# Optimization experiments

Hardware: AMD Instinct MI355X
Metric: run time of the kernel (lower is better)

## Reference

```python
import jax, jax.numpy as jnp
import numpy as np

D_MODEL = 1024
N_HEADS = 16
HEAD_DIM = D_MODEL // N_HEADS


def setup_inputs() -> dict:
    key = jax.random.key(0)
    k1, k2, k3, k4, k5 = jax.random.split(key, 5)
    s = 1.0 / np.sqrt(D_MODEL)
    return {
        "x": jax.random.normal(k1, (2, 2048, D_MODEL), dtype=jnp.float32),
        "w_qkv": jax.random.normal(k2, (D_MODEL, 3 * D_MODEL), dtype=jnp.float32) * s,
        "b_qkv": jax.random.normal(k3, (3 * D_MODEL,), dtype=jnp.float32) * 0.02,
        "w_proj": jax.random.normal(k4, (D_MODEL, D_MODEL), dtype=jnp.float32) * s,
        "b_proj": jax.random.normal(k5, (D_MODEL,), dtype=jnp.float32) * 0.02,
    }


def reference(x, w_qkv, b_qkv, w_proj, b_proj):
    B, S, D = x.shape
    H, Hd = N_HEADS, HEAD_DIM
    qkv = x @ w_qkv + b_qkv                       # [B,S,3D]
    q, k, v = jnp.split(qkv, 3, axis=-1)
    # split heads -> [B,H,S,Hd]
    q = q.reshape(B, S, H, Hd).transpose(0, 2, 1, 3)
    k = k.reshape(B, S, H, Hd).transpose(0, 2, 1, 3)
    v = v.reshape(B, S, H, Hd).transpose(0, 2, 1, 3)
    scale = 1.0 / jnp.sqrt(jnp.asarray(Hd, dtype=x.dtype))
    scores = jnp.einsum("bhqd,bhkd->bhqk", q, k) * scale  # [B,H,S,S]
    causal = jnp.tril(jnp.ones((S, S), dtype=bool))
    scores = jnp.where(causal, scores, jnp.asarray(-jnp.inf, dtype=scores.dtype))
    attn = jax.nn.softmax(scores, axis=-1)
    out = jnp.einsum("bhqk,bhkd->bhqd", attn, v)  # [B,H,S,Hd]
    out = out.transpose(0, 2, 1, 3).reshape(B, S, D)
    return out @ w_proj + b_proj
```

## Files before the change

kernel.cpp:

```cpp
#include <hip/hip_runtime.h>


typedef float f32x4 __attribute__((ext_vector_type(4)));
typedef short bf16x8 __attribute__((ext_vector_type(8)));

#if __has_builtin(__builtin_amdgcn_exp2f)
#define EXP2(x) __builtin_amdgcn_exp2f(x)
#else
#define EXP2(x) exp2f(x)
#endif

__device__ __forceinline__ unsigned short f2bf(float f) {
  union { float f; unsigned u; } v; v.f = f;
  unsigned u = v.u + 0x7fffu + ((v.u >> 16) & 1u);
  return (unsigned short)(u >> 16);
}

__device__ __forceinline__ unsigned pack2bf(float f0, float f1) {
  union { float f; unsigned u; } a, b;
  a.f = f1; b.f = f0;
  return __builtin_amdgcn_perm(a.u + 0x8000u, b.u + 0x8000u, 0x07060302u);
}

__device__ __forceinline__ void async_load16(const void* g, void* lds) {
  __builtin_amdgcn_global_load_lds(
      (const __attribute__((address_space(1))) void*)g,
      (__attribute__((address_space(3))) void*)lds, 16, 0, 0);
}

__global__ void f32_to_bf16_kernel(const float* __restrict__ in,
                                   unsigned short* __restrict__ out, int n) {
  int i = (blockIdx.x * 256 + threadIdx.x) * 4;
  if (i < n) {
    float4 f = *(const float4*)(in + i);
    ushort4 o;
    o.x = f2bf(f.x); o.y = f2bf(f.y); o.z = f2bf(f.z); o.w = f2bf(f.w);
    *(ushort4*)(out + i) = o;
  }
}

__global__ void transpose_f32_bf16_kernel(const float* __restrict__ in,
                                          unsigned short* __restrict__ out,
                                          int K, int N) {
  __shared__ float tile[32][33];
  int n0 = blockIdx.x * 32, k0 = blockIdx.y * 32;
  int tx = threadIdx.x, ty = threadIdx.y;
#pragma unroll
  for (int i = ty; i < 32; i += 8)
    tile[i][tx] = in[(size_t)(k0 + i) * N + (n0 + tx)];
  __syncthreads();
#pragma unroll
  for (int i = ty; i < 32; i += 8)
    out[(size_t)(n0 + i) * K + (k0 + tx)] = f2bf(tile[tx][i]);
}

template <int MI, int NI>
__device__ __forceinline__ void gemm_mainloop(
    const unsigned short* __restrict__ A,
    const unsigned short* __restrict__ BT,
    int K, int mBlk, int nBlk,
    unsigned short* As, unsigned short* Bs,
    f32x4 (&acc)[MI][NI], int lane, int wave)
{
  const int l16 = lane & 15, quad = lane >> 4;
  const int mW = (wave >> 1) * MI * 16;
  const int nW = (wave & 1) * NI * 16;
  constexpr int AROWS = 2 * MI * 16;
  constexpr int BROWS = 2 * NI * 16;
  constexpr int AINST = AROWS / 64;
  constexpr int BINST = BROWS / 64;
  const int rl = lane >> 2;
  const int cl = (lane & 3) * 8;

  for (int k0 = 0; k0 < K; k0 += 32) {
    __syncthreads();
#pragma unroll
    for (int t = 0; t < AINST; ++t) {
      const int rbase = wave * (AROWS / 4) + t * 16;
      async_load16(A + (size_t)(mBlk + rbase + rl) * K + k0 + cl, &As[rbase * 32]);
    }
#pragma unroll
    for (int t = 0; t < BINST; ++t) {
      const int rbase = wave * (BROWS / 4) + t * 16;
      async_load16(BT + (size_t)(nBlk + rbase + rl) * K + k0 + cl, &Bs[rbase * 32]);
    }
    __syncthreads();

    bf16x8 af[MI], bf[NI];
#pragma unroll
    for (int i = 0; i < MI; ++i)
      af[i] = *(const bf16x8*)&As[(mW + i * 16 + l16) * 32 + quad * 8];
#pragma unroll
    for (int j = 0; j < NI; ++j)
      bf[j] = *(const bf16x8*)&Bs[(nW + j * 16 + l16) * 32 + quad * 8];
#pragma unroll
    for (int i = 0; i < MI; ++i)
#pragma unroll
      for (int j = 0; j < NI; ++j)
        acc[i][j] = __builtin_amdgcn_mfma_f32_16x16x32_bf16(af[i], bf[j], acc[i][j], 0, 0, 0);
  }
}

__global__ __launch_bounds__(256) void qkv_gemm_kernel(
    const unsigned short* __restrict__ A,
    const unsigned short* __restrict__ WT,
    const float* __restrict__ bias,
    unsigned short* __restrict__ QKV)
{
  __shared__ unsigned short As[128 * 32];
  __shared__ unsigned short Bs[128 * 32];
  const int lane = threadIdx.x & 63;
  const int wave = threadIdx.x >> 6;
  const int l16 = lane & 15, quad = lane >> 4;

  f32x4 acc[4][4];
  const f32x4 z4 = {0.f, 0.f, 0.f, 0.f};
#pragma unroll
  for (int i = 0; i < 4; ++i)
#pragma unroll
    for (int j = 0; j < 4; ++j) acc[i][j] = z4;

  gemm_mainloop<4, 4>(A, WT, 1024, blockIdx.x * 128, blockIdx.y * 128,
                      As, Bs, acc, lane, wave);

  const int m0 = blockIdx.x * 128 + (wave >> 1) * 64;
  const int n0 = blockIdx.y * 128 + (wave & 1) * 64;
  const int whichW = n0 >> 10;
  const int bb = m0 >> 11;
  const int sBase = (m0 & 2047);
  const size_t planeE = (size_t)2 * 16 * 2048 * 64;

  if (whichW == 2) {
    unsigned short* Vb = QKV + 2 * planeE;
#pragma unroll
    for (int j = 0; j < 4; ++j) {
      const int rem = (n0 & 1023) + j * 16 + l16;
      const int hh = rem >> 6, hd = rem & 63;
      const float bv = bias[n0 + j * 16 + l16];
      unsigned short* col = Vb + (((size_t)bb * 16 + hh) * 64 + hd) * 2048;
#pragma unroll
      for (int i = 0; i < 4; ++i) {
        unsigned short pk[4];
#pragma unroll
        for (int r = 0; r < 4; ++r) pk[r] = f2bf(acc[i][j][r] + bv);
        *(ushort4*)&col[sBase + i * 16 + quad * 4] = *(ushort4*)pk;
      }
    }
  } else {
    const float scale = (whichW == 0) ? 0.18033688011112042f : 1.0f;
#pragma unroll
    for (int j = 0; j < 4; ++j) {
      const int n = n0 + j * 16 + l16;
      const float bv = bias[n];
      const int rem = n & 1023;
      const int hh = rem >> 6, hd = rem & 63;
      unsigned short* pl = QKV + (size_t)whichW * planeE +
                           (((size_t)bb * 16 + hh) * 2048) * 64 + hd;
#pragma unroll
      for (int r = 0; r < 4; ++r) {
        const int s = sBase + (quad * 4 + r);
#pragma unroll
        for (int i = 0; i < 4; ++i)
          pl[(size_t)(s + i * 16) * 64] = f2bf((acc[i][j][r] + bv) * scale);
      }
    }
  }
}

__global__ __launch_bounds__(256) void attn_kernel(
    const unsigned short* __restrict__ QKV,
    unsigned short* __restrict__ AO)
{
  __shared__ __align__(16) unsigned short Ks[3 * 64 * 64];
  __shared__ __align__(16) unsigned short Vs[3 * 64 * 64];
  __shared__ unsigned short Plds[4 * 32 * 72];
  const int lane = threadIdx.x & 63;
  const int wave = threadIdx.x >> 6;
  const int l16 = lane & 15, quad = lane >> 4;
  const int h = blockIdx.y, b = blockIdx.z;
  const int qg = b ? blockIdx.x : (15 - blockIdx.x);
  const int qw = qg * 128 + wave * 32;

  const size_t planeE = (size_t)2 * 16 * 2048 * 64;
  const size_t bhS = ((size_t)b * 16 + h) * (size_t)(2048 * 64);
  const unsigned short* Q   = QKV + bhS;
  const unsigned short* Kg  = QKV + planeE + bhS;
  const unsigned short* VTg = QKV + 2 * planeE + bhS;

  unsigned short* Pw = Plds + wave * (32 * 72);
  const f32x4 z4 = {0.f, 0.f, 0.f, 0.f};

  bf16x8 qf_[2][2];
#pragma unroll
  for (int qf = 0; qf < 2; ++qf)
#pragma unroll
    for (int hf = 0; hf < 2; ++hf)
      qf_[qf][hf] = *(const bf16x8*)(Q + (size_t)(qw + qf * 16 + l16) * 64 + hf * 32 + quad * 8);

  f32x4 O[2][4];
#pragma unroll
  for (int qf = 0; qf < 2; ++qf)
#pragma unroll
    for (int f = 0; f < 4; ++f) O[qf][f] = z4;
  float lpa[2] = {0.f, 0.f}, lpb[2] = {0.f, 0.f};

  const int tbase = (wave & 1) * 4;
  const bool doV = wave >= 2;
  const int sw7 = l16 & 7;

  auto stage = [&](int tileIdx, int bufIdx) {
    const int kt = tileIdx * 64;
    unsigned short* Kb = Ks + bufIdx * 4096;
    unsigned short* Vb = Vs + bufIdx * 4096;
#pragma unroll
    for (int i = 0; i < 4; ++i) {
      const int t = tbase + i;
      const int s = t * 64 + lane;
      const int row = s >> 3;
      const int c = (s & 7) ^ (row & 7);
      if (doV)
        async_load16(VTg + (size_t)row * 2048 + kt + c * 8, Vb + t * 512);
      else
        async_load16(Kg + (size_t)(kt + row) * 64 + c * 8, Kb + t * 512);
    }
  };

  const int nt = qg * 2 + 2;
  stage(0, 0);
  stage(1, 1);
  for (int ti = 0; ti < nt; ++ti) {
    asm volatile("s_waitcnt vmcnt(4)\n\ts_barrier" ::: "memory");
    const int tn = (ti + 2 < nt) ? ti + 2 : nt - 1;
    stage(tn, (ti + 2) % 3);
    const int kt = ti * 64;
    const unsigned short* Kb = Ks + (ti % 3) * 4096;
    const unsigned short* Vb = Vs + (ti % 3) * 4096;

    if (kt <= qw + 31) {
      const bool dmask = (kt + 63 > qw);
      f32x4 sc[4][2];
#pragma unroll
      for (int kg = 0; kg < 4; ++kg) {
        const int row = kg * 16 + l16;
        bf16x8 ka0 = *(const bf16x8*)&Kb[(row * 8 + (quad ^ sw7)) * 8];
        bf16x8 ka1 = *(const bf16x8*)&Kb[(row * 8 + ((4 + quad) ^ sw7)) * 8];
#pragma unroll
        for (int qf = 0; qf < 2; ++qf) {
          f32x4 s0 = z4;
          s0 = __builtin_amdgcn_mfma_f32_16x16x32_bf16(ka0, qf_[qf][0], s0, 0, 0, 0);
          s0 = __builtin_amdgcn_mfma_f32_16x16x32_bf16(ka1, qf_[qf][1], s0, 0, 0, 0);
          sc[kg][qf] = s0;
        }
      }

#pragma unroll
      for (int kg = 0; kg < 4; ++kg)
#pragma unroll
        for (int qf = 0; qf < 2; ++qf) {
          float p[4];
#pragma unroll
          for (int r = 0; r < 4; ++r) {
            float v = sc[kg][qf][r];
            if (dmask) {
              const int key = kt + kg * 16 + quad * 4 + r;
              const int q = qw + qf * 16 + l16;
              if (key > q) v = -INFINITY;
            }
            p[r] = EXP2(v);
          }
          lpa[qf] += p[0] + p[1];
          lpb[qf] += p[2] + p[3];
          uint2 pk;
          pk.x = pack2bf(p[0], p[1]);
          pk.y = pack2bf(p[2], p[3]);
          *(uint2*)&Pw[(qf * 16 + l16) * 72 + kg * 16 + quad * 4] = pk;
        }
      asm volatile("s_waitcnt lgkmcnt(0)" ::: "memory");

#pragma unroll
      for (int ks = 0; ks < 2; ++ks) {
        bf16x8 pa[2];
#pragma unroll
        for (int qf = 0; qf < 2; ++qf)
          pa[qf] = *(const bf16x8*)&Pw[(qf * 16 + l16) * 72 + ks * 32 + quad * 8];
#pragma unroll
        for (int f = 0; f < 4; ++f) {
          const int row = f * 16 + l16;
          bf16x8 vb = *(const bf16x8*)&Vb[(row * 8 + ((ks * 4 + quad) ^ sw7)) * 8];
#pragma unroll
          for (int qf = 0; qf < 2; ++qf)
            O[qf][f] = __builtin_amdgcn_mfma_f32_16x16x32_bf16(pa[qf], vb, O[qf][f], 0, 0, 0);
        }
      }
    }
  }

  float lp[2] = {lpa[0] + lpb[0], lpa[1] + lpb[1]};
#pragma unroll
  for (int qf = 0; qf < 2; ++qf) {
    lp[qf] += __shfl_xor(lp[qf], 16, 64);
    lp[qf] += __shfl_xor(lp[qf], 32, 64);
  }

#pragma unroll
  for (int qf = 0; qf < 2; ++qf) {
    float inv[4];
#pragma unroll
    for (int r = 0; r < 4; ++r)
      inv[r] = 1.0f / __shfl(lp[qf], quad * 4 + r, 64);
    unsigned short* op = AO + ((size_t)b * 2048 + qw + qf * 16 + quad * 4) * 1024 + h * 64 + l16;
#pragma unroll
    for (int f = 0; f < 4; ++f)
#pragma unroll
      for (int r = 0; r < 4; ++r)
        op[(size_t)r * 1024 + f * 16] = f2bf(O[qf][f][r] * inv[r]);
  }
}

__global__ __launch_bounds__(256) void proj_gemm_kernel(
    const unsigned short* __restrict__ A,
    const unsigned short* __restrict__ WT,
    const float* __restrict__ bias,
    float* __restrict__ out)
{
  __shared__ unsigned short As[64 * 32];
  __shared__ unsigned short Bs[128 * 32];
  const int lane = threadIdx.x & 63;
  const int wave = threadIdx.x >> 6;
  const int l16 = lane & 15, quad = lane >> 4;

  f32x4 acc[2][4];
  const f32x4 z4 = {0.f, 0.f, 0.f, 0.f};
#pragma unroll
  for (int i = 0; i < 2; ++i)
#pragma unroll
    for (int j = 0; j < 4; ++j) acc[i][j] = z4;

  gemm_mainloop<2, 4>(A, WT, 1024, blockIdx.x * 64, blockIdx.y * 128,
                      As, Bs, acc, lane, wave);

  const int m0 = blockIdx.x * 64 + (wave >> 1) * 32;
  const int n0 = blockIdx.y * 128 + (wave & 1) * 64;
#pragma unroll
  for (int i = 0; i < 2; ++i) {
#pragma unroll
    for (int j = 0; j < 4; ++j) {
      const int n = n0 + j * 16 + l16;
      const float bv = bias[n];
#pragma unroll
      for (int r = 0; r < 4; ++r) {
        const int m = m0 + i * 16 + quad * 4 + r;
        out[(size_t)m * 1024 + n] = acc[i][j][r] + bv;
      }
    }
  }
}

extern "C" void kernel_launch(void* const* d_in, const int* in_sizes, int n_in,
                              void* d_out, int out_size, void* d_ws, size_t ws_size,
                              hipStream_t stream) {
  const float* x      = (const float*)d_in[0];
  const float* w_qkv  = (const float*)d_in[1];
  const float* b_qkv  = (const float*)d_in[2];
  const float* w_proj = (const float*)d_in[3];
  const float* b_proj = (const float*)d_in[4];
  float* out = (float*)d_out;

  unsigned short* Xb  = (unsigned short*)d_ws;
  unsigned short* WTq = Xb + (size_t)4096 * 1024;
  unsigned short* WTp = WTq + (size_t)3072 * 1024;
  unsigned short* QKV = WTp + (size_t)1024 * 1024;
  unsigned short* AO  = QKV + (size_t)3 * 4096 * 1024;

  f32_to_bf16_kernel<<<4096, 256, 0, stream>>>(x, Xb, 4096 * 1024);
  transpose_f32_bf16_kernel<<<dim3(96, 32), dim3(32, 8), 0, stream>>>(w_qkv, WTq, 1024, 3072);
  transpose_f32_bf16_kernel<<<dim3(32, 32), dim3(32, 8), 0, stream>>>(w_proj, WTp, 1024, 1024);
  qkv_gemm_kernel<<<dim3(32, 24), 256, 0, stream>>>(Xb, WTq, b_qkv, QKV);
  attn_kernel<<<dim3(16, 16, 2), 256, 0, stream>>>(QKV, AO);
  proj_gemm_kernel<<<dim3(64, 8), 256, 0, stream>>>(AO, WTp, b_proj, out);
}
```

Baseline: 204.0 us.

## Rewrite attention inner loop with 32x32 MFMA, register-resident P via permlane swap

The attention kernel now uses 32x32x16 bf16 MFMAs instead of 16x16x32 for both the QK^T scores and the PV accumulation. The probability tile is converted with v_cvt_pk_bf16_f32 and rearranged across lanes with v_permlane32_swap, so it no longer round-trips through an LDS scratch buffer. The softmax denominator is accumulated by an extra MFMA against a ones vector rather than scalar adds and shuffles, and s_setprio plus launch_bounds(256,2) are added. This removes LDS traffic and a wait per tile, at the cost of an extra MFMA per key chunk and higher register pressure from the 16-wide accumulators.

```diff
diff --git a/kernel.cpp b/kernel.cpp
--- a/kernel.cpp
+++ b/kernel.cpp
@@ -2,6 +2,7 @@
 
 
 typedef float f32x4 __attribute__((ext_vector_type(4)));
+typedef float f32x16 __attribute__((ext_vector_type(16)));
 typedef short bf16x8 __attribute__((ext_vector_type(8)));
 
 #if __has_builtin(__builtin_amdgcn_exp2f)
@@ -14,12 +15,6 @@
   union { float f; unsigned u; } v; v.f = f;
   unsigned u = v.u + 0x7fffu + ((v.u >> 16) & 1u);
   return (unsigned short)(u >> 16);
-}
-
-__device__ __forceinline__ unsigned pack2bf(float f0, float f1) {
-  union { float f; unsigned u; } a, b;
-  a.f = f1; b.f = f0;
-  return __builtin_amdgcn_perm(a.u + 0x8000u, b.u + 0x8000u, 0x07060302u);
 }
 
 __device__ __forceinline__ void async_load16(const void* g, void* lds) {
@@ -167,16 +162,16 @@
   }
 }
 
-__global__ __launch_bounds__(256) void attn_kernel(
+__global__ __launch_bounds__(256, 2) void attn_kernel(
     const unsigned short* __restrict__ QKV,
     unsigned short* __restrict__ AO)
 {
   __shared__ __align__(16) unsigned short Ks[3 * 64 * 64];
   __shared__ __align__(16) unsigned short Vs[3 * 64 * 64];
-  __shared__ unsigned short Plds[4 * 32 * 72];
   const int lane = threadIdx.x & 63;
   const int wave = threadIdx.x >> 6;
-  const int l16 = lane & 15, quad = lane >> 4;
+  const int l31 = lane & 31;
+  const int hi  = lane >> 5;
   const int h = blockIdx.y, b = blockIdx.z;
   const int qg = b ? blockIdx.x : (15 - blockIdx.x);
   const int qw = qg * 128 + wave * 32;
@@ -187,26 +182,21 @@
   const unsigned short* Kg  = QKV + planeE + bhS;
   const unsigned short* VTg = QKV + 2 * planeE + bhS;
 
-  unsigned short* Pw = Plds + wave * (32 * 72);
-  const f32x4 z4 = {0.f, 0.f, 0.f, 0.f};
-
-  bf16x8 qf_[2][2];
-#pragma unroll
-  for (int qf = 0; qf < 2; ++qf)
-#pragma unroll
-    for (int hf = 0; hf < 2; ++hf)
-      qf_[qf][hf] = *(const bf16x8*)(Q + (size_t)(qw + qf * 16 + l16) * 64 + hf * 32 + quad * 8);
-
-  f32x4 O[2][4];
-#pragma unroll
-  for (int qf = 0; qf < 2; ++qf)
-#pragma unroll
-    for (int f = 0; f < 4; ++f) O[qf][f] = z4;
-  float lpa[2] = {0.f, 0.f}, lpb[2] = {0.f, 0.f};
+  bf16x8 qf_[4];
+#pragma unroll
+  for (int t = 0; t < 4; ++t)
+    qf_[t] = *(const bf16x8*)(Q + (size_t)(qw + l31) * 64 + t * 16 + hi * 8);
+
+  bf16x8 onesf;
+#pragma unroll
+  for (int i = 0; i < 8; ++i) onesf[i] = (short)0x3F80;
+
+  f32x16 O[2], Osum;
+#pragma unroll
+  for (int r = 0; r < 16; ++r) { O[0][r] = 0.f; O[1][r] = 0.f; Osum[r] = 0.f; }
 
   const int tbase = (wave & 1) * 4;
   const bool doV = wave >= 2;
-  const int sw7 = l16 & 7;
 
   auto stage = [&](int tileIdx, int bufIdx) {
     const int kt = tileIdx * 64;
@@ -238,82 +228,72 @@
 
     if (kt <= qw + 31) {
       const bool dmask = (kt + 63 > qw);
-      f32x4 sc[4][2];
-#pragma unroll
-      for (int kg = 0; kg < 4; ++kg) {
-        const int row = kg * 16 + l16;
-        bf16x8 ka0 = *(const bf16x8*)&Kb[(row * 8 + (quad ^ sw7)) * 8];
-        bf16x8 ka1 = *(const bf16x8*)&Kb[(row * 8 + ((4 + quad) ^ sw7)) * 8];
-#pragma unroll
-        for (int qf = 0; qf < 2; ++qf) {
-          f32x4 s0 = z4;
-          s0 = __builtin_amdgcn_mfma_f32_16x16x32_bf16(ka0, qf_[qf][0], s0, 0, 0, 0);
-          s0 = __builtin_amdgcn_mfma_f32_16x16x32_bf16(ka1, qf_[qf][1], s0, 0, 0, 0);
-          sc[kg][qf] = s0;
+#pragma unroll
+      for (int kg = 0; kg < 2; ++kg) {
+        const int krow = kg * 32 + l31;
+        const int ks7 = krow & 7;
+        bf16x8 ka[4];
+#pragma unroll
+        for (int t = 0; t < 4; ++t)
+          ka[t] = *(const bf16x8*)&Kb[(krow * 8 + ((t * 2 + hi) ^ ks7)) * 8];
+
+        f32x16 sc;
+#pragma unroll
+        for (int r = 0; r < 16; ++r) sc[r] = 0.f;
+        __builtin_amdgcn_s_setprio(1);
+#pragma unroll
+        for (int t = 0; t < 4; ++t)
+          sc = __builtin_amdgcn_mfma_f32_32x32x16_bf16(ka[t], qf_[t], sc, 0, 0, 0);
+        __builtin_amdgcn_s_setprio(0);
+
+        float p[16];
+#pragma unroll
+        for (int r = 0; r < 16; ++r) {
+          float v = sc[r];
+          if (dmask) {
+            const int key = kt + kg * 32 + (r & 3) + 8 * (r >> 2) + 4 * hi;
+            if (key > qw + l31) v = -INFINITY;
+          }
+          p[r] = EXP2(v);
+        }
+        unsigned c8[8];
+#pragma unroll
+        for (int i = 0; i < 8; ++i)
+          asm("v_cvt_pk_bf16_f32 %0, %1, %2"
+              : "=v"(c8[i]) : "v"(p[2 * i]), "v"(p[2 * i + 1]));
+
+#pragma unroll
+        for (int half = 0; half < 2; ++half) {
+          unsigned a0 = c8[4 * half + 0], a1 = c8[4 * half + 1];
+          unsigned a2 = c8[4 * half + 2], a3 = c8[4 * half + 3];
+          asm("v_permlane32_swap_b32 %0, %1" : "+v"(a0), "+v"(a2));
+          asm("v_permlane32_swap_b32 %0, %1" : "+v"(a1), "+v"(a3));
+          union { unsigned u[4]; bf16x8 v; } pa;
+          pa.u[0] = a0; pa.u[1] = a1; pa.u[2] = a2; pa.u[3] = a3;
+          const int kc = kg * 2 + half;
+
+          __builtin_amdgcn_s_setprio(1);
+          Osum = __builtin_amdgcn_mfma_f32_32x32x16_bf16(pa.v, onesf, Osum, 0, 0, 0);
+#pragma unroll
+          for (int g = 0; g < 2; ++g) {
+            const int vrow = g * 32 + l31;
+            bf16x8 vb = *(const bf16x8*)&Vb[(vrow * 8 + ((kc * 2 + hi) ^ (vrow & 7))) * 8];
+            O[g] = __builtin_amdgcn_mfma_f32_32x32x16_bf16(pa.v, vb, O[g], 0, 0, 0);
+          }
+          __builtin_amdgcn_s_setprio(0);
         }
       }
-
-#pragma unroll
-      for (int kg = 0; kg < 4; ++kg)
-#pragma unroll
-        for (int qf = 0; qf < 2; ++qf) {
-          float p[4];
-#pragma unroll
-          for (int r = 0; r < 4; ++r) {
-            float v = sc[kg][qf][r];
-            if (dmask) {
-              const int key = kt + kg * 16 + quad * 4 + r;
-              const int q = qw + qf * 16 + l16;
-              if (key > q) v = -INFINITY;
-            }
-            p[r] = EXP2(v);
-          }
-          lpa[qf] += p[0] + p[1];
-          lpb[qf] += p[2] + p[3];
-          uint2 pk;
-          pk.x = pack2bf(p[0], p[1]);
-          pk.y = pack2bf(p[2], p[3]);
-          *(uint2*)&Pw[(qf * 16 + l16) * 72 + kg * 16 + quad * 4] = pk;
-        }
-      asm volatile("s_waitcnt lgkmcnt(0)" ::: "memory");
-
-#pragma unroll
-      for (int ks = 0; ks < 2; ++ks) {
-        bf16x8 pa[2];
-#pragma unroll
-        for (int qf = 0; qf < 2; ++qf)
-          pa[qf] = *(const bf16x8*)&Pw[(qf * 16 + l16) * 72 + ks * 32 + quad * 8];
-#pragma unroll
-        for (int f = 0; f < 4; ++f) {
-          const int row = f * 16 + l16;
-          bf16x8 vb = *(const bf16x8*)&Vb[(row * 8 + ((ks * 4 + quad) ^ sw7)) * 8];
-#pragma unroll
-          for (int qf = 0; qf < 2; ++qf)
-            O[qf][f] = __builtin_amdgcn_mfma_f32_16x16x32_bf16(pa[qf], vb, O[qf][f], 0, 0, 0);
-        }
-      }
-    }
-  }
-
-  float lp[2] = {lpa[0] + lpb[0], lpa[1] + lpb[1]};
-#pragma unroll
-  for (int qf = 0; qf < 2; ++qf) {
-    lp[qf] += __shfl_xor(lp[qf], 16, 64);
-    lp[qf] += __shfl_xor(lp[qf], 32, 64);
-  }
-
-#pragma unroll
-  for (int qf = 0; qf < 2; ++qf) {
-    float inv[4];
-#pragma unroll
-    for (int r = 0; r < 4; ++r)
-      inv[r] = 1.0f / __shfl(lp[qf], quad * 4 + r, 64);
-    unsigned short* op = AO + ((size_t)b * 2048 + qw + qf * 16 + quad * 4) * 1024 + h * 64 + l16;
-#pragma unroll
-    for (int f = 0; f < 4; ++f)
-#pragma unroll
-      for (int r = 0; r < 4; ++r)
-        op[(size_t)r * 1024 + f * 16] = f2bf(O[qf][f][r] * inv[r]);
+    }
+  }
+
+  unsigned short* base = AO + ((size_t)b * 2048 + qw) * 1024 + h * 64 + l31;
+#pragma unroll
+  for (int r = 0; r < 16; ++r) {
+    const float inv = 1.0f / Osum[r];
+    const int row = (r & 3) + 8 * (r >> 2) + 4 * hi;
+#pragma unroll
+    for (int g = 0; g < 2; ++g)
+      base[(size_t)row * 1024 + g * 32] = f2bf(O[g][r] * inv);
   }
 }
 
```

After: 201.8 us. Within noise of the previous version (-1.1%).
